# Kernel optimization log

Hardware: AMD Instinct MI355X
Metric: run time of the kernel (lower is better)

Reference implementation:

```python
import jax, jax.numpy as jnp
import numpy as np

UNITS = 1024
IN_DIM = 1024
BATCH = 4096


def setup_inputs() -> dict:
    key = jax.random.key(0)
    ks = jax.random.split(key, 11)
    C = UNITS + IN_DIM  # concat dim
    glorot = lambda k, shp: jax.random.uniform(k, shp, jnp.float32, -1.0, 1.0) * np.sqrt(6.0 / (shp[0] + shp[1]))
    return {
        "inputs": jax.random.normal(ks[0], (BATCH, IN_DIM), jnp.float32),
        "hidden_state": jax.random.normal(ks[1], (BATCH, UNITS), jnp.float32),
        "cell_state": jax.random.normal(ks[2], (BATCH, UNITS), jnp.float32),
        "W_f": glorot(ks[3], (C, UNITS)), "b_f": jnp.ones((UNITS,), jnp.float32),  # forget bias init = ones
        "W_i": glorot(ks[4], (C, UNITS)), "b_i": jnp.zeros((UNITS,), jnp.float32),
        "W_c": glorot(ks[5], (C, UNITS)), "b_c": jnp.zeros((UNITS,), jnp.float32),
        "W_o": glorot(ks[6], (C, UNITS)), "b_o": jnp.zeros((UNITS,), jnp.float32),
    }


def reference(inputs, hidden_state, cell_state, W_f, b_f, W_i, b_i, W_c, b_c, W_o, b_o):
    # concat order matches original: (hidden_state, inputs)
    x = jnp.concatenate((hidden_state, inputs), axis=1)  # [B, U+D]
    f = jax.nn.sigmoid(x @ W_f + b_f)
    i = jax.nn.sigmoid(x @ W_i + b_i)
    c_cand = jnp.tanh(x @ W_c + b_c)
    new_cell = f * cell_state + i * c_cand
    o = jax.nn.sigmoid(x @ W_o + b_o)
    new_hidden = o * jnp.tanh(new_cell)
    return (new_hidden, new_cell)
```

## Files before the change

### kernel.cpp

```cpp
#include <hip/hip_runtime.h>
#include <hip/hip_bf16.h>

#define BATCH  4096
#define UNITS  1024
#define CDIM   2048
#define NDIM   4096

typedef __attribute__((ext_vector_type(8))) short bf16x8;
typedef __attribute__((ext_vector_type(4))) short bf16x4;
typedef __attribute__((ext_vector_type(4))) float f32x4;

__device__ __forceinline__ void gload_lds16(const void* g, void* l) {
    __builtin_amdgcn_global_load_lds(
        (const __attribute__((address_space(1))) unsigned int*)g,
        (__attribute__((address_space(3))) unsigned int*)l, 16, 0, 0);
}

__device__ __forceinline__ float sigm(float x) { return 1.f / (1.f + __expf(-x)); }
__device__ __forceinline__ float tanh_fast(float x) { return 2.f / (1.f + __expf(-2.f * x)) - 1.f; }

__device__ __forceinline__ short f2bf(float f) {
    __hip_bfloat16 h = __float2bfloat16(f);
    return *reinterpret_cast<short*>(&h);
}

__global__ __launch_bounds__(256) void prep(
        const float* __restrict__ h, const float* __restrict__ in,
        const float* __restrict__ Wf, const float* __restrict__ Wi,
        const float* __restrict__ Wc, const float* __restrict__ Wo,
        __hip_bfloat16* __restrict__ x, __hip_bfloat16* __restrict__ Wt) {
    __shared__ float lds[64 * 65];
    int b = blockIdx.x, tid = threadIdx.x;
    if (b < 4096) {
        int t   = b * 256 + tid;
        int row = t >> 8;
        int c8  = (t & 255) << 3;
        const float* src = (c8 < UNITS) ? (h + (size_t)row * UNITS + c8)
                                        : (in + (size_t)row * UNITS + (c8 - UNITS));
        float4 v0 = ((const float4*)src)[0];
        float4 v1 = ((const float4*)src)[1];
        bf16x8 o;
        o[0] = f2bf(v0.x); o[1] = f2bf(v0.y); o[2] = f2bf(v0.z); o[3] = f2bf(v0.w);
        o[4] = f2bf(v1.x); o[5] = f2bf(v1.y); o[6] = f2bf(v1.z); o[7] = f2bf(v1.w);
        *(bf16x8*)(x + (size_t)row * CDIM + c8) = o;
    } else {
        int idx = b - 4096;
        int g = idx >> 9, kt = (idx >> 4) & 31, ut = idx & 15;
        const float* W = (g == 0) ? Wf : (g == 1) ? Wi : (g == 2) ? Wc : Wo;
        int k0 = kt * 64, u0 = ut * 64;
        int r16 = tid & 15, hi = tid >> 4;
#pragma unroll
        for (int it = 0; it < 4; ++it) {
            int kl = it * 16 + hi;
            float4 v = *(const float4*)&W[(size_t)(k0 + kl) * UNITS + u0 + r16 * 4];
            float* d = &lds[kl * 65 + r16 * 4];
            d[0] = v.x; d[1] = v.y; d[2] = v.z; d[3] = v.w;
        }
        __syncthreads();
#pragma unroll
        for (int it = 0; it < 4; ++it) {
            int ul = it * 16 + hi;
            int u  = u0 + ul;
            int n  = ((u >> 5) << 7) + (((u >> 4) & 1) << 6) + (g << 4) + (u & 15);
            bf16x4 o;
#pragma unroll
            for (int j = 0; j < 4; ++j) o[j] = f2bf(lds[(r16 * 4 + j) * 65 + ul]);
            *(bf16x4*)(Wt + (size_t)n * CDIM + k0 + r16 * 4) = o;
        }
    }
}

__global__ __launch_bounds__(512, 2) void gemm_lstm(
    const __hip_bfloat16* __restrict__ A,
    const __hip_bfloat16* __restrict__ Bt,
    const float* __restrict__ b_f, const float* __restrict__ b_i,
    const float* __restrict__ b_c, const float* __restrict__ b_o,
    const float* __restrict__ cell,
    float* __restrict__ out)
{
    extern __shared__ short smem[];
    const int K = CDIM;

    int bid = blockIdx.x;
    int nb  = (bid & 7) * 2 + ((bid >> 3) & 1);
    int mb  = bid >> 4;
    int m0  = mb * 256, n0 = nb * 256;

    int tid  = threadIdx.x;
    int w    = tid >> 6, lane = tid & 63;
    int wm   = w >> 2, wn2 = w & 3;
    int quad = lane >> 4, r16 = lane & 15;

    f32x4 acc[8][4];
#pragma unroll
    for (int i = 0; i < 8; ++i)
#pragma unroll
        for (int j = 0; j < 4; ++j) acc[i][j] = (f32x4){0.f, 0.f, 0.f, 0.f};

    const short* Ag0 = (const short*)A  + (size_t)(m0)       * K;
    const short* Ag1 = (const short*)A  + (size_t)(m0 + 128) * K;
    const short* Bg0 = (const short*)Bt + (size_t)(n0)       * K;
    const short* Bg1 = (const short*)Bt + (size_t)(n0 + 128) * K;

    short* lds = smem;
    unsigned SB  = (unsigned)(size_t)(__attribute__((address_space(3))) short*)smem;
    unsigned kc0 = (unsigned)((quad ^ (r16 & 7)) * 16);
    unsigned kc1 = (unsigned)(((quad + 4) ^ (r16 & 7)) * 16);
    unsigned aA  = SB + wm * 16384 + r16 * 128;
    unsigned aB  = SB + 65536 + wn2 * 8192 + r16 * 128;

    bf16x8 bfr[4];

#define STG(SRC, DSTOFF, KT)                                                   \
    { _Pragma("unroll")                                                        \
      for (int q_ = 0; q_ < 2; ++q_) {                                         \
          int s_ = q_ * 512 + tid;                                             \
          int row_ = s_ >> 3, cg_ = (s_ & 7) ^ (row_ & 7);                     \
          gload_lds16(SRC + (size_t)row_ * K + (KT) * 64 + cg_ * 8,            \
                      lds + (DSTOFF) + s_ * 8);                                \
      } }

#define DSR(DST, ADDR, OFFTXT)                                                 \
    asm volatile("ds_read_b128 %0, %1 " OFFTXT : "=v"(DST) : "v"(ADDR) : "memory");

#define PHASE(P, KS, IH, STAGE_CODE, WAIT_CODE)                                \
    {                                                                          \
        unsigned adA_ = aA + (P) * 32768 + ((KS) ? kc1 : kc0);                 \
        bf16x8 af0, af1, af2, af3;                                             \
        if ((IH) == 0) {                                                       \
            unsigned adB_ = aB + (P) * 32768 + ((KS) ? kc1 : kc0);             \
            DSR(af0, adA_, "")                                                 \
            DSR(af1, adA_, "offset:2048")                                      \
            DSR(af2, adA_, "offset:4096")                                      \
            DSR(af3, adA_, "offset:6144")                                      \
            DSR(bfr[0], adB_, "")                                              \
            DSR(bfr[1], adB_, "offset:2048")                                   \
            DSR(bfr[2], adB_, "offset:4096")                                   \
            DSR(bfr[3], adB_, "offset:6144")                                   \
        } else {                                                               \
            DSR(af0, adA_, "offset:8192")                                      \
            DSR(af1, adA_, "offset:10240")                                     \
            DSR(af2, adA_, "offset:12288")                                     \
            DSR(af3, adA_, "offset:14336")                                     \
        }                                                                      \
        STAGE_CODE;                                                            \
        asm volatile("s_barrier" ::: "memory");                                \
        asm volatile("s_waitcnt lgkmcnt(0)" ::: "memory");                     \
        __builtin_amdgcn_sched_barrier(0);                                     \
        __builtin_amdgcn_s_setprio(1);                                         \
        _Pragma("unroll")                                                      \
        for (int j_ = 0; j_ < 4; ++j_) {                                       \
            acc[(IH)*4+0][j_] = __builtin_amdgcn_mfma_f32_16x16x32_bf16(af0, bfr[j_], acc[(IH)*4+0][j_], 0, 0, 0); \
            acc[(IH)*4+1][j_] = __builtin_amdgcn_mfma_f32_16x16x32_bf16(af1, bfr[j_], acc[(IH)*4+1][j_], 0, 0, 0); \
            acc[(IH)*4+2][j_] = __builtin_amdgcn_mfma_f32_16x16x32_bf16(af2, bfr[j_], acc[(IH)*4+2][j_], 0, 0, 0); \
            acc[(IH)*4+3][j_] = __builtin_amdgcn_mfma_f32_16x16x32_bf16(af3, bfr[j_], acc[(IH)*4+3][j_], 0, 0, 0); \
        }                                                                      \
        __builtin_amdgcn_s_setprio(0);                                         \
        __builtin_amdgcn_sched_barrier(0);                                     \
        WAIT_CODE;                                                             \
        asm volatile("s_barrier" ::: "memory");                                \
    }

#define VM4 asm volatile("s_waitcnt vmcnt(4)" ::: "memory")
#define VM0 asm volatile("s_waitcnt vmcnt(0)" ::: "memory")
#define NOPX ((void)0)

    STG(Ag0, 0,     0)
    STG(Ag1, 8192,  0)
    STG(Bg0, 32768, 0)
    STG(Bg1, 40960, 0)
    STG(Bg0, 49152, 1)
    STG(Bg1, 57344, 1)
    VM4;
    asm volatile("s_barrier" ::: "memory");

    for (int u = 0; u < 15; ++u) {
        int t1 = 2 * u + 1, t2 = 2 * u + 2, t3 = 2 * u + 3;
        PHASE(0, 0, 0, STG(Ag0, 16384, t1), NOPX)
        PHASE(0, 0, 1, STG(Ag1, 24576, t1), NOPX)
        PHASE(0, 1, 0, NOPX, NOPX)
        PHASE(0, 1, 1, STG(Bg0, 32768, t2) STG(Bg1, 40960, t2), VM4)
        PHASE(1, 0, 0, STG(Ag0, 0,     t2), NOPX)
        PHASE(1, 0, 1, STG(Ag1, 8192,  t2), NOPX)
        PHASE(1, 1, 0, NOPX, NOPX)
        PHASE(1, 1, 1, STG(Bg0, 49152, t3) STG(Bg1, 57344, t3), VM4)
    }
    PHASE(0, 0, 0, STG(Ag0, 16384, 31), NOPX)
    PHASE(0, 0, 1, STG(Ag1, 24576, 31), NOPX)
    PHASE(0, 1, 0, NOPX, NOPX)
    PHASE(0, 1, 1, NOPX, VM0)
    PHASE(1, 0, 0, NOPX, NOPX)
    PHASE(1, 0, 1, NOPX, NOPX)
    PHASE(1, 1, 0, NOPX, NOPX)
    PHASE(1, 1, 1, NOPX, NOPX)

#undef PHASE
#undef DSR
#undef STG
#undef VM4
#undef VM0
#undef NOPX

    int uo = nb * 64 + (wn2 >> 1) * 32 + (wn2 & 1) * 16 + r16;
    float bfv = b_f[uo], biv = b_i[uo], bcv = b_c[uo], bov = b_o[uo];
    float* out_h = out;
    float* out_c = out + (size_t)BATCH * UNITS;
#pragma unroll
    for (int i = 0; i < 8; ++i) {
#pragma unroll
        for (int rr = 0; rr < 4; ++rr) {
            int m = m0 + wm * 128 + i * 16 + quad * 4 + rr;
            float fg = sigm(acc[i][0][rr] + bfv);
            float ig = sigm(acc[i][1][rr] + biv);
            float cc = tanh_fast(acc[i][2][rr] + bcv);
            float og = sigm(acc[i][3][rr] + bov);
            float cold = cell[(size_t)m * UNITS + uo];
            float cn = fg * cold + ig * cc;
            out_h[(size_t)m * UNITS + uo] = og * tanh_fast(cn);
            out_c[(size_t)m * UNITS + uo] = cn;
        }
    }
}

extern "C" void kernel_launch(void* const* d_in, const int* in_sizes, int n_in,
                              void* d_out, int out_size, void* d_ws, size_t ws_size,
                              hipStream_t stream) {
    const float* inputs = (const float*)d_in[0];
    const float* hidden = (const float*)d_in[1];
    const float* cell   = (const float*)d_in[2];
    const float* Wf = (const float*)d_in[3];
    const float* bf_ = (const float*)d_in[4];
    const float* Wi = (const float*)d_in[5];
    const float* bi_ = (const float*)d_in[6];
    const float* Wc = (const float*)d_in[7];
    const float* bc_ = (const float*)d_in[8];
    const float* Wo = (const float*)d_in[9];
    const float* bo_ = (const float*)d_in[10];
    float* out = (float*)d_out;

    char* ws = (char*)d_ws;
    __hip_bfloat16* x  = (__hip_bfloat16*)ws;
    __hip_bfloat16* Wt = (__hip_bfloat16*)(ws + (16u << 20));

    static bool attr_set = false;
    if (!attr_set) {
        hipFuncSetAttribute(reinterpret_cast<const void*>(gemm_lstm),
                            hipFuncAttributeMaxDynamicSharedMemorySize, 131072);
        attr_set = true;
    }

    prep<<<dim3(6144), dim3(256), 0, stream>>>(hidden, inputs, Wf, Wi, Wc, Wo, x, Wt);
    gemm_lstm<<<dim3(256), dim3(512), 131072, stream>>>(
        x, Wt, bf_, bi_, bc_, bo_, cell, out);
}
```

Baseline: 199.1 us.

## Double-buffer LDS fragment registers to overlap reads with MFMA

Introduces two register sets each for the A and B fragments. Each phase issues the LDS reads for the next phase's fragments before running its own MFMA block, so LDS latency is hidden behind matrix math instead of being waited on ahead of every MFMA group. The global-load wait moves to the start of the phase, before the barrier, and the first fragments are loaded in a prologue. This adds VGPR pressure from the extra fragment registers and needs careful ordering of barriers against the staged buffers.

```diff
diff --git a/kernel.cpp b/kernel.cpp
--- a/kernel.cpp
+++ b/kernel.cpp
@@ -109,7 +109,8 @@
     unsigned aA  = SB + wm * 16384 + r16 * 128;
     unsigned aB  = SB + 65536 + wn2 * 8192 + r16 * 128;
 
-    bf16x8 bfr[4];
+    bf16x8 afX0, afX1, afX2, afX3, afY0, afY1, afY2, afY3;
+    bf16x8 bfM0, bfM1, bfM2, bfM3, bfN0, bfN1, bfN2, bfN3;
 
 #define STG(SRC, DSTOFF, KT)                                                   \
     { _Pragma("unroll")                                                        \
@@ -123,41 +124,38 @@
 #define DSR(DST, ADDR, OFFTXT)                                                 \
     asm volatile("ds_read_b128 %0, %1 " OFFTXT : "=v"(DST) : "v"(ADDR) : "memory");
 
-#define PHASE(P, KS, IH, STAGE_CODE, WAIT_CODE)                                \
+#define FRAGA0(S, PB, KC) { unsigned a_ = aA + (PB) * 32768 + (KC);            \
+    DSR(af##S##0, a_, "")              DSR(af##S##1, a_, "offset:2048")        \
+    DSR(af##S##2, a_, "offset:4096")   DSR(af##S##3, a_, "offset:6144") }
+#define FRAGA1(S, PB, KC) { unsigned a_ = aA + (PB) * 32768 + (KC);            \
+    DSR(af##S##0, a_, "offset:8192")   DSR(af##S##1, a_, "offset:10240")       \
+    DSR(af##S##2, a_, "offset:12288")  DSR(af##S##3, a_, "offset:14336") }
+#define FRAGB(S, PB, KC) { unsigned b_ = aB + (PB) * 32768 + (KC);             \
+    DSR(bf##S##0, b_, "")              DSR(bf##S##1, b_, "offset:2048")        \
+    DSR(bf##S##2, b_, "offset:4096")   DSR(bf##S##3, b_, "offset:6144") }
+
+#define MFJ(UA, BREG, IH, J)                                                   \
+    acc[(IH)*4+0][J] = __builtin_amdgcn_mfma_f32_16x16x32_bf16(af##UA##0, BREG, acc[(IH)*4+0][J], 0, 0, 0); \
+    acc[(IH)*4+1][J] = __builtin_amdgcn_mfma_f32_16x16x32_bf16(af##UA##1, BREG, acc[(IH)*4+1][J], 0, 0, 0); \
+    acc[(IH)*4+2][J] = __builtin_amdgcn_mfma_f32_16x16x32_bf16(af##UA##2, BREG, acc[(IH)*4+2][J], 0, 0, 0); \
+    acc[(IH)*4+3][J] = __builtin_amdgcn_mfma_f32_16x16x32_bf16(af##UA##3, BREG, acc[(IH)*4+3][J], 0, 0, 0);
+
+#define PHASE(UA, UB, IH, FRAGCODE, STAGECODE, WAITCODE)                       \
     {                                                                          \
-        unsigned adA_ = aA + (P) * 32768 + ((KS) ? kc1 : kc0);                 \
-        bf16x8 af0, af1, af2, af3;                                             \
-        if ((IH) == 0) {                                                       \
-            unsigned adB_ = aB + (P) * 32768 + ((KS) ? kc1 : kc0);             \
-            DSR(af0, adA_, "")                                                 \
-            DSR(af1, adA_, "offset:2048")                                      \
-            DSR(af2, adA_, "offset:4096")                                      \
-            DSR(af3, adA_, "offset:6144")                                      \
-            DSR(bfr[0], adB_, "")                                              \
-            DSR(bfr[1], adB_, "offset:2048")                                   \
-            DSR(bfr[2], adB_, "offset:4096")                                   \
-            DSR(bfr[3], adB_, "offset:6144")                                   \
-        } else {                                                               \
-            DSR(af0, adA_, "offset:8192")                                      \
-            DSR(af1, adA_, "offset:10240")                                     \
-            DSR(af2, adA_, "offset:12288")                                     \
-            DSR(af3, adA_, "offset:14336")                                     \
-        }                                                                      \
-        STAGE_CODE;                                                            \
+        STAGECODE;                                                             \
+        WAITCODE;                                                              \
         asm volatile("s_barrier" ::: "memory");                                \
         asm volatile("s_waitcnt lgkmcnt(0)" ::: "memory");                     \
         __builtin_amdgcn_sched_barrier(0);                                     \
+        FRAGCODE;                                                              \
+        __builtin_amdgcn_sched_barrier(0);                                     \
         __builtin_amdgcn_s_setprio(1);                                         \
-        _Pragma("unroll")                                                      \
-        for (int j_ = 0; j_ < 4; ++j_) {                                       \
-            acc[(IH)*4+0][j_] = __builtin_amdgcn_mfma_f32_16x16x32_bf16(af0, bfr[j_], acc[(IH)*4+0][j_], 0, 0, 0); \
-            acc[(IH)*4+1][j_] = __builtin_amdgcn_mfma_f32_16x16x32_bf16(af1, bfr[j_], acc[(IH)*4+1][j_], 0, 0, 0); \
-            acc[(IH)*4+2][j_] = __builtin_amdgcn_mfma_f32_16x16x32_bf16(af2, bfr[j_], acc[(IH)*4+2][j_], 0, 0, 0); \
-            acc[(IH)*4+3][j_] = __builtin_amdgcn_mfma_f32_16x16x32_bf16(af3, bfr[j_], acc[(IH)*4+3][j_], 0, 0, 0); \
-        }                                                                      \
+        MFJ(UA, bf##UB##0, IH, 0)                                              \
+        MFJ(UA, bf##UB##1, IH, 1)                                              \
+        MFJ(UA, bf##UB##2, IH, 2)                                              \
+        MFJ(UA, bf##UB##3, IH, 3)                                              \
         __builtin_amdgcn_s_setprio(0);                                         \
         __builtin_amdgcn_sched_barrier(0);                                     \
-        WAIT_CODE;                                                             \
         asm volatile("s_barrier" ::: "memory");                                \
     }
 
@@ -173,28 +171,34 @@
     STG(Bg1, 57344, 1)
     VM4;
     asm volatile("s_barrier" ::: "memory");
+    FRAGA0(X, 0, kc0)
+    FRAGB(M, 0, kc0)
 
     for (int u = 0; u < 15; ++u) {
         int t1 = 2 * u + 1, t2 = 2 * u + 2, t3 = 2 * u + 3;
-        PHASE(0, 0, 0, STG(Ag0, 16384, t1), NOPX)
-        PHASE(0, 0, 1, STG(Ag1, 24576, t1), NOPX)
-        PHASE(0, 1, 0, NOPX, NOPX)
-        PHASE(0, 1, 1, STG(Bg0, 32768, t2) STG(Bg1, 40960, t2), VM4)
-        PHASE(1, 0, 0, STG(Ag0, 0,     t2), NOPX)
-        PHASE(1, 0, 1, STG(Ag1, 8192,  t2), NOPX)
-        PHASE(1, 1, 0, NOPX, NOPX)
-        PHASE(1, 1, 1, STG(Bg0, 49152, t3) STG(Bg1, 57344, t3), VM4)
-    }
-    PHASE(0, 0, 0, STG(Ag0, 16384, 31), NOPX)
-    PHASE(0, 0, 1, STG(Ag1, 24576, 31), NOPX)
-    PHASE(0, 1, 0, NOPX, NOPX)
-    PHASE(0, 1, 1, NOPX, VM0)
-    PHASE(1, 0, 0, NOPX, NOPX)
-    PHASE(1, 0, 1, NOPX, NOPX)
-    PHASE(1, 1, 0, NOPX, NOPX)
-    PHASE(1, 1, 1, NOPX, NOPX)
+        PHASE(X, M, 0, FRAGA1(Y, 0, kc0),                   STG(Ag0, 16384, t1), NOPX)
+        PHASE(Y, M, 1, FRAGA0(X, 0, kc1) FRAGB(N, 0, kc1),  STG(Ag1, 24576, t1), NOPX)
+        PHASE(X, N, 0, FRAGA1(Y, 0, kc1),                   NOPX, NOPX)
+        PHASE(Y, N, 1, FRAGA0(X, 1, kc0) FRAGB(M, 1, kc0),  STG(Bg0, 32768, t2) STG(Bg1, 40960, t2), VM4)
+        PHASE(X, M, 0, FRAGA1(Y, 1, kc0),                   STG(Ag0, 0,     t2), NOPX)
+        PHASE(Y, M, 1, FRAGA0(X, 1, kc1) FRAGB(N, 1, kc1),  STG(Ag1, 8192,  t2), NOPX)
+        PHASE(X, N, 0, FRAGA1(Y, 1, kc1),                   NOPX, NOPX)
+        PHASE(Y, N, 1, FRAGA0(X, 0, kc0) FRAGB(M, 0, kc0),  STG(Bg0, 49152, t3) STG(Bg1, 57344, t3), VM4)
+    }
+    PHASE(X, M, 0, FRAGA1(Y, 0, kc0),                   STG(Ag0, 16384, 31), NOPX)
+    PHASE(Y, M, 1, FRAGA0(X, 0, kc1) FRAGB(N, 0, kc1),  STG(Ag1, 24576, 31), NOPX)
+    PHASE(X, N, 0, FRAGA1(Y, 0, kc1),                   NOPX, NOPX)
+    PHASE(Y, N, 1, FRAGA0(X, 1, kc0) FRAGB(M, 1, kc0),  NOPX, VM0)
+    PHASE(X, M, 0, FRAGA1(Y, 1, kc0),                   NOPX, NOPX)
+    PHASE(Y, M, 1, FRAGA0(X, 1, kc1) FRAGB(N, 1, kc1),  NOPX, NOPX)
+    PHASE(X, N, 0, FRAGA1(Y, 1, kc1),                   NOPX, NOPX)
+    PHASE(Y, N, 1, NOPX,                                NOPX, NOPX)
 
 #undef PHASE
+#undef MFJ
+#undef FRAGA0
+#undef FRAGA1
+#undef FRAGB
 #undef DSR
 #undef STG
 #undef VM4
```

After: 198.5 us. About the same (-0.3%).
